# Kernel optimization log

Hardware: AMD Instinct MI355X
Metric: run time of the kernel (lower is better)

## Reference

```python
import jax, jax.numpy as jnp
import numpy as np
import math

D_MODEL = 384
N_HEADS = 3
D_K = D_MODEL // N_HEADS  # 128
LN_EPS = 1e-6


def entmax15(z, axis=-1):
    """Exact 1.5-entmax (Peters et al. 2019), sort-based."""
    z = z / 2.0
    z = z - jnp.max(z, axis=axis, keepdims=True)
    zs = -jnp.sort(-z, axis=axis)                      # descending
    K = z.shape[axis]
    rho = jnp.arange(1, K + 1, dtype=z.dtype)          # broadcasts on last axis
    mean = jnp.cumsum(zs, axis=axis) / rho
    mean_sq = jnp.cumsum(zs * zs, axis=axis) / rho
    ss = rho * (mean_sq - mean * mean)
    delta = (1.0 - ss) / rho
    tau = mean - jnp.sqrt(jnp.clip(delta, 0.0))
    support = jnp.sum(tau <= zs, axis=axis, keepdims=True)  # support size
    tau_star = jnp.take_along_axis(tau, support - 1, axis=axis)
    p = jnp.clip(z - tau_star, 0.0)
    return p * p


def layer_norm(x, a, b):
    # matches torch module: std with Bessel correction (unbiased), eps added to std
    mean = jnp.mean(x, axis=-1, keepdims=True)
    n = x.shape[-1]
    var = jnp.sum((x - mean) ** 2, axis=-1, keepdims=True) / (n - 1)
    std = jnp.sqrt(var)
    return a * (x - mean) / (std + LN_EPS) + b


def setup_inputs() -> dict:
    key = jax.random.key(0)
    ks = jax.random.split(key, 8)
    B, N = 2, 2048
    scale = 1.0 / math.sqrt(D_MODEL)
    x = jax.random.normal(ks[0], (B, D_MODEL, N), dtype=jnp.float32)
    wq = jax.random.uniform(ks[1], (D_MODEL, D_MODEL), jnp.float32, -scale, scale)
    bq = jax.random.uniform(ks[2], (D_MODEL,), jnp.float32, -scale, scale)
    wk = jax.random.uniform(ks[3], (D_MODEL, D_MODEL), jnp.float32, -scale, scale)
    bk = jax.random.uniform(ks[4], (D_MODEL,), jnp.float32, -scale, scale)
    wv = jax.random.uniform(ks[5], (D_MODEL, D_MODEL), jnp.float32, -scale, scale)
    bv = jax.random.uniform(ks[6], (D_MODEL,), jnp.float32, -scale, scale)
    ln_a = jnp.ones((D_MODEL,), jnp.float32)
    ln_b = jnp.ones((D_MODEL,), jnp.float32)
    return {"x": x, "wq": wq, "bq": bq, "wk": wk, "bk": bk,
            "wv": wv, "bv": bv, "ln_a": ln_a, "ln_b": ln_b}


def reference(x, wq, bq, wk, bk, wv, bv, ln_a, ln_b):
    B = x.shape[0]
    xt = jnp.transpose(x, (0, 2, 1))                   # [B, N, C]
    x1 = xt

    def proj(w, b):
        y = jnp.einsum('bnc,oc->bno', xt, w) + b       # [B, N, C]
        return jnp.transpose(y.reshape(B, -1, N_HEADS, D_K), (0, 2, 1, 3))

    q = proj(wq, bq)                                   # [B, h, N, d_k]
    k = proj(wk, bk)
    v = proj(wv, bv)

    energy = jnp.einsum('bhqd,bhkd->bhqk', q, k) / math.sqrt(D_K)
    attn = entmax15(energy, axis=-1)                   # sparse attention weights
    out = jnp.einsum('bhqk,bhkd->bhqd', attn, v)       # [B, h, N, d_k]
    out = jnp.transpose(out, (0, 2, 1, 3)).reshape(B, -1, N_HEADS * D_K)
    # dropout layers are identity in eval mode
    return x1 + layer_norm(out, ln_a, ln_b)
```

## Files before the change

kernel.cpp:

```cpp
#include <hip/hip_runtime.h>
#include <hip/hip_fp16.h>
#include <math.h>

#define DM   384
#define NH   3
#define DK   128
#define NSEQ 2048
#define BATCH 2
#define NTOK (BATCH*NSEQ)
#define SEG  (BATCH*NSEQ*DM)
#define NEWTON_IT 6
#define QT   16
#define ZP   520

typedef __attribute__((ext_vector_type(8))) short     bf16x8;
typedef __attribute__((ext_vector_type(4))) float     f32x4;
typedef __attribute__((ext_vector_type(8))) _Float16  h8;
typedef __attribute__((ext_vector_type(4))) _Float16  h4;
typedef __attribute__((ext_vector_type(2))) _Float16  h2v;

#if __has_builtin(__builtin_amdgcn_fdot2)
#define HAVE_FDOT2 1
#else
#define HAVE_FDOT2 0
#endif

typedef const unsigned int __attribute__((address_space(1)))* gas1_t;
typedef unsigned int __attribute__((address_space(3)))* las3_t;
__device__ __forceinline__ void gll16(const void* g, void* l) {
  __builtin_amdgcn_global_load_lds((gas1_t)g, (las3_t)l, 16, 0, 0);
}

__device__ __forceinline__ unsigned short f2bf(float f) {
  unsigned u = __builtin_bit_cast(unsigned, f);
  u += 0x7FFFu + ((u >> 16) & 1u);
  return (unsigned short)(u >> 16);
}

__global__ __launch_bounds__(256) void transpose_k(const float* __restrict__ x,
                                                   float* __restrict__ xT,
                                                   unsigned short* __restrict__ xbf) {
  __shared__ float tile[32][33];
  int b  = blockIdx.z;
  int cB = blockIdx.y * 32;
  int nB = blockIdx.x * 32;
  int tx = threadIdx.x & 31, ty = threadIdx.x >> 5;
#pragma unroll
  for (int i = 0; i < 4; i++)
    tile[ty + i*8][tx] = x[((size_t)b*DM + cB + ty + i*8)*NSEQ + nB + tx];
  __syncthreads();
#pragma unroll
  for (int i = 0; i < 4; i++) {
    float v = tile[tx][ty + i*8];
    size_t row = (size_t)b*NSEQ + nB + ty + i*8;
    xT [row*DM + cB + tx] = v;
    xbf[row*DM + cB + tx] = f2bf(v);
  }
}

__global__ __launch_bounds__(256) void wconv_k(const float* __restrict__ wq,
    const float* __restrict__ wk, const float* __restrict__ wv,
    unsigned short* __restrict__ wbf) {
  int pj = blockIdx.y;
  const float* src = (pj == 0) ? wq : (pj == 1) ? wk : wv;
  int i = (blockIdx.x * 256 + threadIdx.x) * 4;
  float4 v = *(const float4*)(src + i);
  ushort4 o;
  o.x = f2bf(v.x); o.y = f2bf(v.y); o.z = f2bf(v.z); o.w = f2bf(v.w);
  *(ushort4*)(wbf + (size_t)pj*DM*DM + i) = o;
}

__global__ __launch_bounds__(256) void proj_mfma_k(
    const unsigned short* __restrict__ xbf,
    const unsigned short* __restrict__ wbf,
    const float* __restrict__ bq, const float* __restrict__ bk, const float* __restrict__ bv,
    unsigned short* __restrict__ Qo, unsigned short* __restrict__ Ko,
    unsigned short* __restrict__ VTo) {
  int tid = threadIdx.x, lane = tid & 63, w = tid >> 6;
  int g = lane >> 4, li = lane & 15;
  int wr = w >> 1, wc = w & 1;
  int h  = blockIdx.y;
  int pj = blockIdx.z;
  const unsigned short* wp0 = wbf + (size_t)pj * DM * DM;
  const float* bias = (pj == 0) ? bq : (pj == 1) ? bk : bv;

  const unsigned short *Am, *Bn;
  int mB, nB;
  if (pj < 2) { Am = wp0; mB = h*128 + wr*64;          Bn = xbf; nB = blockIdx.x*128 + wc*64; }
  else        { Am = xbf; mB = blockIdx.x*128 + wr*64; Bn = wp0; nB = h*128 + wc*64; }

  f32x4 acc[4][4];
#pragma unroll
  for (int fi = 0; fi < 4; fi++)
#pragma unroll
    for (int fj = 0; fj < 4; fj++) acc[fi][fj] = (f32x4){0.f, 0.f, 0.f, 0.f};

#pragma unroll 2
  for (int ks = 0; ks < DM/32; ks++) {
    bf16x8 af[4], bf[4];
#pragma unroll
    for (int fi = 0; fi < 4; fi++)
      af[fi] = *(const bf16x8*)(Am + (size_t)(mB + fi*16 + li)*DM + ks*32 + g*8);
#pragma unroll
    for (int fj = 0; fj < 4; fj++)
      bf[fj] = *(const bf16x8*)(Bn + (size_t)(nB + fj*16 + li)*DM + ks*32 + g*8);
#pragma unroll
    for (int fi = 0; fi < 4; fi++)
#pragma unroll
      for (int fj = 0; fj < 4; fj++)
        acc[fi][fj] = __builtin_amdgcn_mfma_f32_16x16x32_bf16(af[fi], bf[fj], acc[fi][fj], 0, 0, 0);
  }

  if (pj < 2) {
    unsigned short* dst = (pj == 0) ? Qo : Ko;
#pragma unroll
    for (int fi = 0; fi < 4; fi++) {
      int o0 = mB + fi*16 + g*4;
      float4 bb = *(const float4*)(bias + o0);
      int d0 = o0 & 127;
#pragma unroll
      for (int fj = 0; fj < 4; fj++) {
        int tok = nB + fj*16 + li;
        int bb_ = tok >> 11, n = tok & 2047;
        ushort4 v4;
        v4.x = f2bf(acc[fi][fj][0] + bb.x);
        v4.y = f2bf(acc[fi][fj][1] + bb.y);
        v4.z = f2bf(acc[fi][fj][2] + bb.z);
        v4.w = f2bf(acc[fi][fj][3] + bb.w);
        *(ushort4*)(dst + ((size_t)(bb_*NH + h)*NSEQ + n)*DK + d0) = v4;
      }
    }
  } else {
#pragma unroll
    for (int fj = 0; fj < 4; fj++) {
      int o  = nB + fj*16 + li;
      float bb = bias[o];
      int d  = o & 127;
#pragma unroll
      for (int fi = 0; fi < 4; fi++) {
        int tok0 = mB + fi*16 + g*4;
        int bb_ = tok0 >> 11, n0 = tok0 & 2047;
        ushort4 v4;
        v4.x = __builtin_bit_cast(unsigned short, (_Float16)(acc[fi][fj][0] + bb));
        v4.y = __builtin_bit_cast(unsigned short, (_Float16)(acc[fi][fj][1] + bb));
        v4.z = __builtin_bit_cast(unsigned short, (_Float16)(acc[fi][fj][2] + bb));
        v4.w = __builtin_bit_cast(unsigned short, (_Float16)(acc[fi][fj][3] + bb));
        *(ushort4*)(VTo + ((size_t)(bb_*NH + h)*DK + d)*NSEQ + n0) = v4;
      }
    }
  }
}

__device__ __forceinline__ void scan16(const h2v* zh, float tau,
                                       float& f, float& g, float& c) {
  float ff = 0.f, gg = 0.f, cc = 0.f;
#if HAVE_FDOT2
  _Float16 th = (_Float16)tau;
  h2v t2 = {th, th};
  h2v zero2 = {(_Float16)0.f, (_Float16)0.f};
  h2v one2  = {(_Float16)1.f, (_Float16)1.f};
  h2v big2  = {(_Float16)60000.f, (_Float16)60000.f};
#pragma unroll
  for (int i = 0; i < 16; i++) {
    h2v d = __builtin_elementwise_max(zh[i] - t2, zero2);
    ff = __builtin_amdgcn_fdot2(d, d, ff, false);
    gg = __builtin_amdgcn_fdot2(d, one2, gg, false);
    h2v mm = __builtin_elementwise_min(d * big2, one2);
    cc = __builtin_amdgcn_fdot2(mm, one2, cc, false);
  }
#else
#pragma unroll
  for (int i = 0; i < 16; i++) {
#pragma unroll
    for (int j = 0; j < 2; j++) {
      float z = (float)zh[i][j];
      float d = fmaxf(z - tau, 0.f);
      ff = fmaf(d, d, ff);
      gg += d;
      cc += (d > 0.f) ? 1.f : 0.f;
    }
  }
#endif
  f = ff; g = gg; c = cc;
}

__device__ __forceinline__ float nstep(float tau, float f, float g, float c, float m) {
  float num  = f - 1.0f;
  float disc = fmaxf(g*g - c*num, 0.f);
  float den  = (num >= 0.f) ? (g + sqrtf(disc)) : (2.0f * g);
  float t = tau + num / fmaxf(den, 1e-12f);
  return fminf(t, m - 0.01f);
}

__global__ __launch_bounds__(256, 3) void attn_k(const unsigned short* __restrict__ Qb,
    const unsigned short* __restrict__ Kb, const _Float16* __restrict__ VTb,
    float* __restrict__ AO) {
  __shared__ _Float16 stg[2][8192];
  __shared__ _Float16 zbuf[QT * ZP];

  int tid = threadIdx.x, lane = tid & 63, w = tid >> 6;
  int g = lane >> 4, li = lane & 15;
  int swz = (blockIdx.x & 7) * 96 + (blockIdx.x >> 3);
  int bh = swz / (NSEQ/QT), qb = swz % (NSEQ/QT);
  int qbase = qb * QT;
  const unsigned short* Qh  = Qb  + (size_t)bh * NSEQ * DK;
  const unsigned short* Kh  = Kb  + (size_t)bh * NSEQ * DK;
  const _Float16*       VTh = VTb + (size_t)bh * DK * NSEQ;
  const float zs = 0.044194173824159216f;

  bf16x8 bq[4];
#pragma unroll
  for (int ks = 0; ks < 4; ks++)
    bq[ks] = *(const bf16x8*)(Qh + (size_t)(qbase + li)*DK + ks*32 + g*8);

  auto stageK = [&](int c, int s, int b) {
#pragma unroll
    for (int j = 0; j < 4; j++) {
      int idx   = (j*4 + w)*64 + lane;
      int row_l = idx >> 4;
      int ch    = idx & 15;
      const unsigned short* src = Kh + (size_t)(c*512 + s*64 + row_l)*DK
                                     + ((ch ^ (row_l & 7)) * 8);
      void* dst = (void*)((char*)&stg[b][0] + (size_t)(j*4 + w) * 1024);
      gll16(src, dst);
    }
  };
  auto stageV = [&](int c, int s, int b) {
#pragma unroll
    for (int j = 0; j < 4; j++) {
      int idx = (j*4 + w)*64 + lane;
      int dr  = idx >> 3;
      int ch  = idx & 7;
      const _Float16* src = VTh + (size_t)dr*NSEQ + c*512 + s*64
                                + ((ch ^ (dr & 7)) * 8);
      void* dst = (void*)((char*)&stg[b][0] + (size_t)(j*4 + w) * 1024);
      gll16(src, dst);
    }
  };

  h8 zr[4][4];
#pragma unroll
  for (int c = 0; c < 4; c++) {
    stageK(c, 0, 0);
    __syncthreads();
    for (int s = 0; s < 8; s++) {
      if (s < 7) stageK(c, s + 1, (s + 1) & 1);
      const _Float16* kb = &stg[s & 1][0];
      bf16x8 bk[4];
#pragma unroll
      for (int ks = 0; ks < 4; ks++)
        bk[ks] = *(const bf16x8*)(kb + (size_t)(w*16 + li)*128
                                     + (((ks*4 + g) ^ (li & 7)) * 8));
      f32x4 za = (f32x4){0.f,0.f,0.f,0.f};
#pragma unroll
      for (int ks = 0; ks < 4; ks++)
        za = __builtin_amdgcn_mfma_f32_16x16x32_bf16(bk[ks], bq[ks], za, 0, 0, 0);
      h4 p;
#pragma unroll
      for (int r = 0; r < 4; r++) p[r] = (_Float16)(za[r] * zs);
      *(h4*)(zbuf + (size_t)li*ZP + s*64 + w*16 + g*4) = p;
      __syncthreads();
    }
#pragma unroll
    for (int r = 0; r < 4; r++)
      zr[r][c] = *(const h8*)(zbuf + (size_t)(w*4 + r)*ZP + lane*8);
    __syncthreads();
  }

  float tau[4], mx[4];
#pragma unroll
  for (int r = 0; r < 4; r++) {
    union { h8 v[4]; h2v h[16]; } u;
#pragma unroll
    for (int c = 0; c < 4; c++) u.v[c] = zr[r][c];
    h2v m2 = u.h[0];
#pragma unroll
    for (int i = 1; i < 16; i++) m2 = __builtin_elementwise_max(m2, u.h[i]);
    float m = fmaxf((float)m2[0], (float)m2[1]);
#pragma unroll
    for (int off = 32; off > 0; off >>= 1) m = fmaxf(m, __shfl_xor(m, off));
    mx[r] = m;
    tau[r] = m - 1.0f;
  }
  for (int it = 0; it < NEWTON_IT; ++it) {
    float f[4], gg[4], cc[4];
#pragma unroll
    for (int r = 0; r < 4; r++) {
      union { h8 v[4]; h2v h[16]; } ur;
#pragma unroll
      for (int c = 0; c < 4; c++) ur.v[c] = zr[r][c];
      scan16(ur.h, tau[r], f[r], gg[r], cc[r]);
    }
#pragma unroll
    for (int off = 32; off > 0; off >>= 1) {
#pragma unroll
      for (int r = 0; r < 4; r++) {
        f[r]  += __shfl_xor(f[r],  off);
        gg[r] += __shfl_xor(gg[r], off);
        cc[r] += __shfl_xor(cc[r], off);
      }
    }
#pragma unroll
    for (int r = 0; r < 4; r++) tau[r] = nstep(tau[r], f[r], gg[r], cc[r], mx[r]);
  }

  f32x4 pacc[2];
  pacc[0] = (f32x4){0.f,0.f,0.f,0.f};
  pacc[1] = (f32x4){0.f,0.f,0.f,0.f};
#pragma unroll
  for (int c = 0; c < 4; c++) {
#pragma unroll
    for (int r = 0; r < 4; r++) {
      union { h8 v; h2v h[4]; } u;
      u.v = zr[r][c];
      _Float16 th = (_Float16)tau[r];
      h2v t2 = {th, th};
      h2v zero2 = {(_Float16)0.f, (_Float16)0.f};
#pragma unroll
      for (int j = 0; j < 4; j++) {
        h2v d = __builtin_elementwise_max(u.h[j] - t2, zero2);
        u.h[j] = d * d;
      }
      *(h8*)(zbuf + (size_t)(w*4 + r)*ZP + lane*8) = u.v;
    }
    stageV(c, 0, 0);
    __syncthreads();
    for (int s = 0; s < 8; s++) {
      if (s < 7) stageV(c, s + 1, (s + 1) & 1);
      const _Float16* vb = &stg[s & 1][0];
#pragma unroll
      for (int k2 = 0; k2 < 2; k2++) {
        h8 pa = *(const h8*)(zbuf + (size_t)li*ZP + s*64 + k2*32 + g*8);
#pragma unroll
        for (int dt = 0; dt < 2; dt++) {
          int dr = w*32 + dt*16 + li;
          h8 bv = *(const h8*)(vb + (size_t)dr*64 + (((k2*4 + g) ^ (dr & 7)) * 8));
          pacc[dt] = __builtin_amdgcn_mfma_f32_16x16x32_f16(pa, bv, pacc[dt], 0, 0, 0);
        }
      }
      __syncthreads();
    }
  }

  int b = bh / NH, h = bh % NH;
#pragma unroll
  for (int dt = 0; dt < 2; dt++)
#pragma unroll
    for (int r = 0; r < 4; r++)
      AO[((size_t)b*NSEQ + qbase + g*4 + r)*DM + h*DK + w*32 + dt*16 + li] = pacc[dt][r];
}

__global__ __launch_bounds__(256) void ln_k(const float* __restrict__ AO,
    const float* __restrict__ xT, const float* __restrict__ ga,
    const float* __restrict__ gb, float* __restrict__ outp) {
  int lane = threadIdx.x & 63;
  int wave = threadIdx.x >> 6;
  int row  = blockIdx.x * 4 + wave;
  const float* ao = AO + (size_t)row*DM;
  float2 c0 = *(const float2*)(ao + lane*2);
  float2 c1 = *(const float2*)(ao + 128 + lane*2);
  float2 c2 = *(const float2*)(ao + 256 + lane*2);
  float s  = c0.x + c0.y + c1.x + c1.y + c2.x + c2.y;
  float ss = c0.x*c0.x + c0.y*c0.y + c1.x*c1.x + c1.y*c1.y + c2.x*c2.x + c2.y*c2.y;
#pragma unroll
  for (int off = 32; off > 0; off >>= 1) {
    s  += __shfl_xor(s,  off);
    ss += __shfl_xor(ss, off);
  }
  float mean = s * (1.0f / 384.0f);
  float var  = (ss - 384.0f*mean*mean) * (1.0f / 383.0f);
  var = fmaxf(var, 0.f);
  float inv = 1.0f / (sqrtf(var) + 1e-6f);
  const float* xr = xT + (size_t)row*DM;
  float* op = outp + (size_t)row*DM;
#pragma unroll
  for (int ch = 0; ch < 3; ch++) {
    int i0 = ch*128 + lane*2;
    float2 g  = *(const float2*)(ga + i0);
    float2 bb = *(const float2*)(gb + i0);
    float2 xv = *(const float2*)(xr + i0);
    float2 av = (ch == 0) ? c0 : (ch == 1) ? c1 : c2;
    float2 o;
    o.x = g.x*(av.x - mean)*inv + bb.x + xv.x;
    o.y = g.y*(av.y - mean)*inv + bb.y + xv.y;
    *(float2*)(op + i0) = o;
  }
}

extern "C" void kernel_launch(void* const* d_in, const int* in_sizes, int n_in,
                              void* d_out, int out_size, void* d_ws, size_t ws_size,
                              hipStream_t stream) {
  const float* x  = (const float*)d_in[0];
  const float* wq = (const float*)d_in[1];
  const float* bq = (const float*)d_in[2];
  const float* wk = (const float*)d_in[3];
  const float* bk = (const float*)d_in[4];
  const float* wv = (const float*)d_in[5];
  const float* bv = (const float*)d_in[6];
  const float* la = (const float*)d_in[7];
  const float* lb = (const float*)d_in[8];
  float* out = (float*)d_out;

  char* wsb = (char*)d_ws;
  float* xT = (float*)wsb;
  float* AO = (float*)(wsb + (size_t)SEG*4);
  unsigned short* Qb  = (unsigned short*)(wsb + (size_t)SEG*8);
  unsigned short* Kb  = (unsigned short*)(wsb + (size_t)SEG*8 + (size_t)SEG*2);
  unsigned short* VT  = (unsigned short*)(wsb + (size_t)SEG*8 + (size_t)SEG*4);
  unsigned short* xbf = (unsigned short*)(wsb + (size_t)SEG*8 + (size_t)SEG*6);
  unsigned short* wbf = (unsigned short*)(wsb + (size_t)SEG*8 + (size_t)SEG*8);

  hipLaunchKernelGGL(transpose_k, dim3(NSEQ/32, DM/32, BATCH), dim3(256), 0, stream,
                     x, xT, xbf);
  hipLaunchKernelGGL(wconv_k, dim3(DM*DM/1024, 3), dim3(256), 0, stream, wq, wk, wv, wbf);
  hipLaunchKernelGGL(proj_mfma_k, dim3(NTOK/128, NH, 3), dim3(256), 0, stream,
                     xbf, wbf, bq, bk, bv, Qb, Kb, VT);
  hipLaunchKernelGGL(attn_k, dim3(BATCH*NH*(NSEQ/QT)), dim3(256), 0, stream,
                     Qb, Kb, (const _Float16*)VT, AO);
  hipLaunchKernelGGL(ln_k, dim3(BATCH*NSEQ/4), dim3(256), 0, stream, AO, xT, la, lb, out);
}
```

Before: 118.6 us.

## Triple-buffer K/V LDS staging with prefetch distance two and explicit vmcnt waits

```diff
diff --git a/kernel.cpp b/kernel.cpp
--- a/kernel.cpp
+++ b/kernel.cpp
@@ -195,7 +195,7 @@
 __global__ __launch_bounds__(256, 3) void attn_k(const unsigned short* __restrict__ Qb,
     const unsigned short* __restrict__ Kb, const _Float16* __restrict__ VTb,
     float* __restrict__ AO) {
-  __shared__ _Float16 stg[2][8192];
+  __shared__ _Float16 stg[3][8192];
   __shared__ _Float16 zbuf[QT * ZP];
 
   int tid = threadIdx.x, lane = tid & 63, w = tid >> 6;
@@ -212,6 +212,8 @@
 #pragma unroll
   for (int ks = 0; ks < 4; ks++)
     bq[ks] = *(const bf16x8*)(Qh + (size_t)(qbase + li)*DK + ks*32 + g*8);
+  asm volatile("s_waitcnt vmcnt(0)" ::: "memory");
+  __builtin_amdgcn_sched_barrier(0);
 
   auto stageK = [&](int c, int s, int b) {
 #pragma unroll
@@ -221,8 +223,7 @@
       int ch    = idx & 15;
       const unsigned short* src = Kh + (size_t)(c*512 + s*64 + row_l)*DK
                                      + ((ch ^ (row_l & 7)) * 8);
-      void* dst = (void*)((char*)&stg[b][0] + (size_t)(j*4 + w) * 1024);
-      gll16(src, dst);
+      gll16(src, (void*)((char*)&stg[b][0] + (size_t)(j*4 + w) * 1024));
     }
   };
   auto stageV = [&](int c, int s, int b) {
@@ -233,19 +234,25 @@
       int ch  = idx & 7;
       const _Float16* src = VTh + (size_t)dr*NSEQ + c*512 + s*64
                                 + ((ch ^ (dr & 7)) * 8);
-      void* dst = (void*)((char*)&stg[b][0] + (size_t)(j*4 + w) * 1024);
-      gll16(src, dst);
+      gll16(src, (void*)((char*)&stg[b][0] + (size_t)(j*4 + w) * 1024));
     }
   };
 
   h8 zr[4][4];
+  stageK(0, 0, 0);
+  stageK(0, 1, 1);
 #pragma unroll
   for (int c = 0; c < 4; c++) {
-    stageK(c, 0, 0);
-    __syncthreads();
+#pragma unroll
     for (int s = 0; s < 8; s++) {
-      if (s < 7) stageK(c, s + 1, (s + 1) & 1);
-      const _Float16* kb = &stg[s & 1][0];
+      if (s < 6) stageK(c, s + 2, (s + 2) % 3);
+      if (s < 6)       asm volatile("s_waitcnt vmcnt(8)" ::: "memory");
+      else if (s == 6) asm volatile("s_waitcnt vmcnt(4)" ::: "memory");
+      else             asm volatile("s_waitcnt vmcnt(0)" ::: "memory");
+      __builtin_amdgcn_sched_barrier(0);
+      __builtin_amdgcn_s_barrier();
+      __builtin_amdgcn_sched_barrier(0);
+      const _Float16* kb = &stg[s % 3][0];
       bf16x8 bk[4];
 #pragma unroll
       for (int ks = 0; ks < 4; ks++)
@@ -259,8 +266,12 @@
 #pragma unroll
       for (int r = 0; r < 4; r++) p[r] = (_Float16)(za[r] * zs);
       *(h4*)(zbuf + (size_t)li*ZP + s*64 + w*16 + g*4) = p;
-      __syncthreads();
-    }
+      __builtin_amdgcn_sched_barrier(0);
+      __builtin_amdgcn_s_barrier();
+      __builtin_amdgcn_sched_barrier(0);
+    }
+    __syncthreads();
+    if (c < 3) { stageK(c+1, 0, 0); stageK(c+1, 1, 1); }
 #pragma unroll
     for (int r = 0; r < 4; r++)
       zr[r][c] = *(const h8*)(zbuf + (size_t)(w*4 + r)*ZP + lane*8);
@@ -307,6 +318,8 @@
   f32x4 pacc[2];
   pacc[0] = (f32x4){0.f,0.f,0.f,0.f};
   pacc[1] = (f32x4){0.f,0.f,0.f,0.f};
+  stageV(0, 0, 0);
+  stageV(0, 1, 1);
 #pragma unroll
   for (int c = 0; c < 4; c++) {
 #pragma unroll
@@ -323,11 +336,17 @@
       }
       *(h8*)(zbuf + (size_t)(w*4 + r)*ZP + lane*8) = u.v;
     }
-    stageV(c, 0, 0);
     __syncthreads();
+#pragma unroll
     for (int s = 0; s < 8; s++) {
-      if (s < 7) stageV(c, s + 1, (s + 1) & 1);
-      const _Float16* vb = &stg[s & 1][0];
+      if (s < 6) stageV(c, s + 2, (s + 2) % 3);
+      if (s < 6)       asm volatile("s_waitcnt vmcnt(8)" ::: "memory");
+      else if (s == 6) asm volatile("s_waitcnt vmcnt(4)" ::: "memory");
+      else             asm volatile("s_waitcnt vmcnt(0)" ::: "memory");
+      __builtin_amdgcn_sched_barrier(0);
+      __builtin_amdgcn_s_barrier();
+      __builtin_amdgcn_sched_barrier(0);
+      const _Float16* vb = &stg[s % 3][0];
 #pragma unroll
       for (int k2 = 0; k2 < 2; k2++) {
         h8 pa = *(const h8*)(zbuf + (size_t)li*ZP + s*64 + k2*32 + g*8);
@@ -338,8 +357,11 @@
           pacc[dt] = __builtin_amdgcn_mfma_f32_16x16x32_f16(pa, bv, pacc[dt], 0, 0, 0);
         }
       }
-      __syncthreads();
-    }
+      __builtin_amdgcn_sched_barrier(0);
+      __builtin_amdgcn_s_barrier();
+      __builtin_amdgcn_sched_barrier(0);
+    }
+    if (c < 3) { stageV(c+1, 0, 0); stageV(c+1, 1, 1); }
   }
 
   int b = bh / NH, h = bh % NH;
```

After: 127.9 us. +7.8%, slower.
